# Kernel tuning notes

Measured on AMD Instinct MI355X. Metric: run time of the kernel, lower is better.

Reference implementation:

```python
import jax, jax.numpy as jnp
import numpy as np

N, M, D = 8192, 8192, 64


def setup_inputs() -> dict:
    key = jax.random.key(0)
    kx, ky = jax.random.split(key)
    X = jax.random.normal(kx, (N, D), dtype=jnp.float32)
    Y = jax.random.normal(ky, (M, D), dtype=jnp.float32)
    return {"X": X, "Y": Y}


def reference(X, Y):
    # Pairwise Euclidean distances via the |x|^2 + |y|^2 - 2<x,y> identity
    # (avoids materializing the [N, M, D] difference tensor).
    x2 = jnp.sum(X * X, axis=1)[:, None]          # [N, 1]
    y2 = jnp.sum(Y * Y, axis=1)[None, :]          # [1, M]
    d2 = x2 + y2 - 2.0 * (X @ Y.T)                # [N, M]
    d = jnp.sqrt(jnp.maximum(d2, 0.0))            # Euclidean distance matrix
    dis_1 = jnp.mean(jnp.min(d, axis=1))          # avg over X of nearest-in-Y
    dis_2 = jnp.mean(jnp.min(d, axis=0))          # avg over Y of nearest-in-X
    return dis_1 + dis_2
```

## Files before the change

### kernel.cpp

```cpp
#include <hip/hip_runtime.h>
#include <math.h>


#define NROWS 8192
#define DDIM  64
#define ITILES 64
#define SLICES 16
#define CHUNKS 4
#define LSTR 72

typedef __bf16 bf16_t;
typedef bf16_t bf16x8 __attribute__((ext_vector_type(8)));
typedef float  f32x4  __attribute__((ext_vector_type(4)));

__global__ void prep_kernel(const float* __restrict__ X,
                            const float* __restrict__ Y,
                            bf16_t* __restrict__ Xbf, bf16_t* __restrict__ Ybf,
                            float* __restrict__ x2, float* __restrict__ y2,
                            float* __restrict__ out) {
  int t = blockIdx.x * blockDim.x + threadIdx.x;
  int half = t >> 15;
  int r = (t >> 2) & (NROWS - 1);
  int part = t & 3;
  const float* src = half ? Y : X;
  bf16_t* dst = half ? Ybf : Xbf;
  float* sq = half ? y2 : x2;

  const float4* p = (const float4*)(src + r * DDIM + part * 16);
  float4 v0 = p[0], v1 = p[1], v2 = p[2], v3 = p[3];
  float s = 0.f;
  s = fmaf(v0.x, v0.x, s); s = fmaf(v0.y, v0.y, s);
  s = fmaf(v0.z, v0.z, s); s = fmaf(v0.w, v0.w, s);
  s = fmaf(v1.x, v1.x, s); s = fmaf(v1.y, v1.y, s);
  s = fmaf(v1.z, v1.z, s); s = fmaf(v1.w, v1.w, s);
  s = fmaf(v2.x, v2.x, s); s = fmaf(v2.y, v2.y, s);
  s = fmaf(v2.z, v2.z, s); s = fmaf(v2.w, v2.w, s);
  s = fmaf(v3.x, v3.x, s); s = fmaf(v3.y, v3.y, s);
  s = fmaf(v3.z, v3.z, s); s = fmaf(v3.w, v3.w, s);

  bf16x8 h0 = {(bf16_t)v0.x, (bf16_t)v0.y, (bf16_t)v0.z, (bf16_t)v0.w,
               (bf16_t)v1.x, (bf16_t)v1.y, (bf16_t)v1.z, (bf16_t)v1.w};
  bf16x8 h1 = {(bf16_t)v2.x, (bf16_t)v2.y, (bf16_t)v2.z, (bf16_t)v2.w,
               (bf16_t)v3.x, (bf16_t)v3.y, (bf16_t)v3.z, (bf16_t)v3.w};
  *(bf16x8*)&dst[r * DDIM + part * 16] = h0;
  *(bf16x8*)&dst[r * DDIM + part * 16 + 8] = h1;

  s += __shfl_xor(s, 1, 64);
  s += __shfl_xor(s, 2, 64);
  if (part == 0) sq[r] = s;
  if (t == 0) out[0] = 0.f;
}

__global__ __launch_bounds__(256, 2)
void mine_kernel(const bf16_t* __restrict__ Xbf, const bf16_t* __restrict__ Ybf,
                 const float* __restrict__ x2g, const float* __restrict__ y2g,
                 float* __restrict__ rslab, float* __restrict__ cslab) {
  __shared__ bf16_t Ys[2][128 * LSTR];

  const int tid = threadIdx.x;
  const int L = tid & 63;
  const int w = tid >> 6;
  const int lr = L & 15;
  const int q = L >> 4;
  const int rh = w >> 1;
  const int ch = w & 1;
  const int itile = blockIdx.x & (ITILES - 1);
  const int slice = blockIdx.x >> 6;
  const int i0 = itile * 128;
  const int rgb = rh * 64;
  const int cgb = ch * 64;
  const int jbase = slice * (CHUNKS * 128);

  bf16x8 Af[8];
#pragma unroll
  for (int a = 0; a < 4; ++a) {
    int row = i0 + rgb + a * 16 + lr;
#pragma unroll
    for (int h = 0; h < 2; ++h)
      Af[a * 2 + h] = *(const bf16x8*)&Xbf[row * DDIM + h * 32 + q * 8];
  }
  float x2r[16];
#pragma unroll
  for (int a = 0; a < 4; ++a) {
    float4 v = *(const float4*)&x2g[i0 + rgb + a * 16 + q * 4];
    x2r[a * 4 + 0] = v.x; x2r[a * 4 + 1] = v.y;
    x2r[a * 4 + 2] = v.z; x2r[a * 4 + 3] = v.w;
  }
  float y2all[CHUNKS][4];
#pragma unroll
  for (int cc = 0; cc < CHUNKS; ++cc)
#pragma unroll
    for (int b = 0; b < 4; ++b)
      y2all[cc][b] = y2g[jbase + cc * 128 + cgb + b * 16 + lr];

  float rmin[16];
#pragma unroll
  for (int k = 0; k < 16; ++k) rmin[k] = INFINITY;

  bf16x8 Bst[4];
#pragma unroll
  for (int p = 0; p < 4; ++p) {
    int f = p * 256 + tid;
    Bst[p] = *(const bf16x8*)&Ybf[(jbase + (f >> 3)) * DDIM + (f & 7) * 8];
  }
#pragma unroll
  for (int p = 0; p < 4; ++p) {
    int f = p * 256 + tid;
    *(bf16x8*)&Ys[0][(f >> 3) * LSTR + (f & 7) * 8] = Bst[p];
  }
  __syncthreads();

  for (int cc = 0; cc < CHUNKS; ++cc) {
    const bf16_t* Yb = Ys[cc & 1];
    if (cc + 1 < CHUNKS) {
      int j0n = jbase + (cc + 1) * 128;
#pragma unroll
      for (int p = 0; p < 4; ++p) {
        int f = p * 256 + tid;
        Bst[p] = *(const bf16x8*)&Ybf[(j0n + (f >> 3)) * DDIM + (f & 7) * 8];
      }
    }

    f32x4 acc[4][4];
#pragma unroll
    for (int a = 0; a < 4; ++a)
#pragma unroll
      for (int b = 0; b < 4; ++b) acc[a][b] = (f32x4){0.f, 0.f, 0.f, 0.f};

#pragma unroll
    for (int b = 0; b < 4; ++b) {
      bf16x8 B0 = *(const bf16x8*)&Yb[(cgb + b * 16 + lr) * LSTR + q * 8];
      bf16x8 B1 = *(const bf16x8*)&Yb[(cgb + b * 16 + lr) * LSTR + 32 + q * 8];
#pragma unroll
      for (int a = 0; a < 4; ++a) {
        acc[a][b] = __builtin_amdgcn_mfma_f32_16x16x32_bf16(Af[a * 2 + 0], B0, acc[a][b], 0, 0, 0);
        acc[a][b] = __builtin_amdgcn_mfma_f32_16x16x32_bf16(Af[a * 2 + 1], B1, acc[a][b], 0, 0, 0);
      }
    }

    float cmin[4] = {INFINITY, INFINITY, INFINITY, INFINITY};
#pragma unroll
    for (int a = 0; a < 4; ++a)
#pragma unroll
      for (int p = 0; p < 4; ++p) {
        float x2v = x2r[a * 4 + p];
        float rm = rmin[a * 4 + p];
#pragma unroll
        for (int b = 0; b < 4; ++b) {
          float s = acc[a][b][p];
          rm = fminf(rm, fmaf(-2.f, s, y2all[cc][b]));
          cmin[b] = fminf(cmin[b], fmaf(-2.f, s, x2v));
        }
        rmin[a * 4 + p] = rm;
      }
#pragma unroll
    for (int b = 0; b < 4; ++b) {
      cmin[b] = fminf(cmin[b], __shfl_xor(cmin[b], 16, 64));
      cmin[b] = fminf(cmin[b], __shfl_xor(cmin[b], 32, 64));
    }
    float v = cmin[0];
    if (q == 1) v = cmin[1];
    else if (q == 2) v = cmin[2];
    else if (q == 3) v = cmin[3];
    cslab[(itile * 2 + rh) * NROWS + jbase + cc * 128 + cgb + L] = v;

    if (cc + 1 < CHUNKS) {
      bf16_t* Yn = Ys[(cc + 1) & 1];
#pragma unroll
      for (int p = 0; p < 4; ++p) {
        int f = p * 256 + tid;
        *(bf16x8*)&Yn[(f >> 3) * LSTR + (f & 7) * 8] = Bst[p];
      }
      __syncthreads();
    }
  }

#pragma unroll
  for (int a = 0; a < 4; ++a)
#pragma unroll
    for (int p = 0; p < 4; ++p) {
      float v = rmin[a * 4 + p];
      v = fminf(v, __shfl_xor(v, 1, 64));
      v = fminf(v, __shfl_xor(v, 2, 64));
      v = fminf(v, __shfl_xor(v, 4, 64));
      v = fminf(v, __shfl_xor(v, 8, 64));
      if (lr == 0)
        rslab[slice * (NROWS * 2) + (i0 + rgb + a * 16 + q * 4 + p) * 2 + ch] = v;
    }
}

__global__ void finish_kernel(const float* __restrict__ x2,
                              const float* __restrict__ y2,
                              const float* __restrict__ rslab,
                              const float* __restrict__ cslab,
                              float* __restrict__ out) {
  const int b = blockIdx.x;
  const int tid = threadIdx.x;
  if (b < 32) {
    int row = b * 256 + tid;
    float m = INFINITY;
#pragma unroll
    for (int g = 0; g < SLICES; ++g) {
      float2 v = *(const float2*)&rslab[g * (NROWS * 2) + row * 2];
      m = fminf(m, fminf(v.x, v.y));
    }
    float v = sqrtf(fmaxf(x2[row] + m, 0.f)) * (1.0f / 8192.0f);
#pragma unroll
    for (int off = 32; off > 0; off >>= 1) v += __shfl_down(v, off, 64);
    __shared__ float partial[4];
    if ((tid & 63) == 0) partial[tid >> 6] = v;
    __syncthreads();
    if (tid == 0)
      atomicAdd(out, partial[0] + partial[1] + partial[2] + partial[3]);
  } else {
    int j = (b - 32) * 64 + (tid & 63);
    int seg = tid >> 6;
    float m = INFINITY;
#pragma unroll
    for (int k = 0; k < 32; ++k)
      m = fminf(m, cslab[(seg * 32 + k) * NROWS + j]);
    __shared__ float red[4][64];
    red[seg][tid & 63] = m;
    __syncthreads();
    if (tid < 64) {
      float mc = fminf(fminf(red[0][tid], red[1][tid]),
                       fminf(red[2][tid], red[3][tid]));
      float v = sqrtf(fmaxf(y2[j] + mc, 0.f)) * (1.0f / 8192.0f);
#pragma unroll
      for (int off = 32; off > 0; off >>= 1) v += __shfl_down(v, off, 64);
      if (tid == 0) atomicAdd(out, v);
    }
  }
}

extern "C" void kernel_launch(void* const* d_in, const int* in_sizes, int n_in,
                              void* d_out, int out_size, void* d_ws, size_t ws_size,
                              hipStream_t stream) {
  const float* X = (const float*)d_in[0];
  const float* Y = (const float*)d_in[1];
  float* out = (float*)d_out;

  char* wsb = (char*)d_ws;
  bf16_t* Xbf = (bf16_t*)wsb;
  bf16_t* Ybf = (bf16_t*)(wsb + (size_t)NROWS * DDIM * 2);
  float* x2 = (float*)(wsb + 2 * (size_t)NROWS * DDIM * 2);
  float* y2 = x2 + NROWS;
  float* rslab = y2 + NROWS;
  float* cslab = rslab + SLICES * NROWS * 2;

  prep_kernel<<<(2 * NROWS * 4) / 256, 256, 0, stream>>>(X, Y, Xbf, Ybf, x2, y2, out);
  mine_kernel<<<ITILES * SLICES, 256, 0, stream>>>(Xbf, Ybf, x2, y2, rslab, cslab);
  finish_kernel<<<160, 256, 0, stream>>>(x2, y2, rslab, cslab, out);
}
```

Measured before the change: 85.03 us.

## Fuse bf16 conversion and squared norms into the distance kernel, drop prep launch

Removes the separate prep kernel. The mine kernel now reads fp32 X and Y directly, computing the bf16 conversion and squared norms on the fly: X rows go to registers, Y chunks go to a single-buffered LDS tile plus a y2 array. Each block covers 8 column chunks instead of 4, which halves the grid to 512 blocks and halves the rslab slices. The norms are added before the slabs are written, so the finish kernel needs no x2/y2 reads. This saves a launch and the bf16/norm round trip through global memory, but loses the register-prefetch double buffering of Y and redoes the Y conversion in every i-tile block.

```diff
diff --git a/kernel.cpp b/kernel.cpp
--- a/kernel.cpp
+++ b/kernel.cpp
@@ -4,122 +4,99 @@
 
 #define NROWS 8192
 #define DDIM  64
-#define ITILES 64
-#define SLICES 16
-#define CHUNKS 4
+#define CHUNKS 8
 #define LSTR 72
 
 typedef __bf16 bf16_t;
 typedef bf16_t bf16x8 __attribute__((ext_vector_type(8)));
 typedef float  f32x4  __attribute__((ext_vector_type(4)));
 
-__global__ void prep_kernel(const float* __restrict__ X,
-                            const float* __restrict__ Y,
-                            bf16_t* __restrict__ Xbf, bf16_t* __restrict__ Ybf,
-                            float* __restrict__ x2, float* __restrict__ y2,
-                            float* __restrict__ out) {
-  int t = blockIdx.x * blockDim.x + threadIdx.x;
-  int half = t >> 15;
-  int r = (t >> 2) & (NROWS - 1);
-  int part = t & 3;
-  const float* src = half ? Y : X;
-  bf16_t* dst = half ? Ybf : Xbf;
-  float* sq = half ? y2 : x2;
-
-  const float4* p = (const float4*)(src + r * DDIM + part * 16);
-  float4 v0 = p[0], v1 = p[1], v2 = p[2], v3 = p[3];
-  float s = 0.f;
-  s = fmaf(v0.x, v0.x, s); s = fmaf(v0.y, v0.y, s);
-  s = fmaf(v0.z, v0.z, s); s = fmaf(v0.w, v0.w, s);
-  s = fmaf(v1.x, v1.x, s); s = fmaf(v1.y, v1.y, s);
-  s = fmaf(v1.z, v1.z, s); s = fmaf(v1.w, v1.w, s);
-  s = fmaf(v2.x, v2.x, s); s = fmaf(v2.y, v2.y, s);
-  s = fmaf(v2.z, v2.z, s); s = fmaf(v2.w, v2.w, s);
-  s = fmaf(v3.x, v3.x, s); s = fmaf(v3.y, v3.y, s);
-  s = fmaf(v3.z, v3.z, s); s = fmaf(v3.w, v3.w, s);
-
-  bf16x8 h0 = {(bf16_t)v0.x, (bf16_t)v0.y, (bf16_t)v0.z, (bf16_t)v0.w,
-               (bf16_t)v1.x, (bf16_t)v1.y, (bf16_t)v1.z, (bf16_t)v1.w};
-  bf16x8 h1 = {(bf16_t)v2.x, (bf16_t)v2.y, (bf16_t)v2.z, (bf16_t)v2.w,
-               (bf16_t)v3.x, (bf16_t)v3.y, (bf16_t)v3.z, (bf16_t)v3.w};
-  *(bf16x8*)&dst[r * DDIM + part * 16] = h0;
-  *(bf16x8*)&dst[r * DDIM + part * 16 + 8] = h1;
-
-  s += __shfl_xor(s, 1, 64);
-  s += __shfl_xor(s, 2, 64);
-  if (part == 0) sq[r] = s;
-  if (t == 0) out[0] = 0.f;
-}
 
 __global__ __launch_bounds__(256, 2)
-void mine_kernel(const bf16_t* __restrict__ Xbf, const bf16_t* __restrict__ Ybf,
-                 const float* __restrict__ x2g, const float* __restrict__ y2g,
-                 float* __restrict__ rslab, float* __restrict__ cslab) {
-  __shared__ bf16_t Ys[2][128 * LSTR];
+void mine_kernel(const float* __restrict__ X, const float* __restrict__ Y,
+                 float* __restrict__ rslab, float* __restrict__ cslab,
+                 float* __restrict__ out) {
+  __shared__ bf16_t Ys[128 * LSTR];
+  __shared__ float y2s[128];
 
   const int tid = threadIdx.x;
   const int L = tid & 63;
   const int w = tid >> 6;
   const int lr = L & 15;
-  const int q = L >> 4;
-  const int rh = w >> 1;
-  const int ch = w & 1;
-  const int itile = blockIdx.x & (ITILES - 1);
+  const int q  = L >> 4;
+  const int rh = w >> 1, ch = w & 1;
+  const int itile = blockIdx.x & 63;
   const int slice = blockIdx.x >> 6;
   const int i0 = itile * 128;
-  const int rgb = rh * 64;
-  const int cgb = ch * 64;
+  const int rgb = rh * 64, cgb = ch * 64;
   const int jbase = slice * (CHUNKS * 128);
 
+  if (blockIdx.x == 0 && tid == 0) out[0] = 0.f;
+
   bf16x8 Af[8];
-#pragma unroll
-  for (int a = 0; a < 4; ++a) {
-    int row = i0 + rgb + a * 16 + lr;
-#pragma unroll
-    for (int h = 0; h < 2; ++h)
-      Af[a * 2 + h] = *(const bf16x8*)&Xbf[row * DDIM + h * 32 + q * 8];
+  float x2r[16];
+  {
+    float x2acc[4];
+#pragma unroll
+    for (int a = 0; a < 4; ++a) {
+      const float4* rp = (const float4*)(X + (i0 + rgb + a * 16 + lr) * DDIM);
+      float4 u0 = rp[q * 2],     u1 = rp[q * 2 + 1];
+      float4 u2 = rp[8 + q * 2], u3 = rp[8 + q * 2 + 1];
+      float s = 0.f;
+      s = fmaf(u0.x, u0.x, s); s = fmaf(u0.y, u0.y, s);
+      s = fmaf(u0.z, u0.z, s); s = fmaf(u0.w, u0.w, s);
+      s = fmaf(u1.x, u1.x, s); s = fmaf(u1.y, u1.y, s);
+      s = fmaf(u1.z, u1.z, s); s = fmaf(u1.w, u1.w, s);
+      s = fmaf(u2.x, u2.x, s); s = fmaf(u2.y, u2.y, s);
+      s = fmaf(u2.z, u2.z, s); s = fmaf(u2.w, u2.w, s);
+      s = fmaf(u3.x, u3.x, s); s = fmaf(u3.y, u3.y, s);
+      s = fmaf(u3.z, u3.z, s); s = fmaf(u3.w, u3.w, s);
+      Af[a * 2 + 0] = (bf16x8){(bf16_t)u0.x, (bf16_t)u0.y, (bf16_t)u0.z, (bf16_t)u0.w,
+                               (bf16_t)u1.x, (bf16_t)u1.y, (bf16_t)u1.z, (bf16_t)u1.w};
+      Af[a * 2 + 1] = (bf16x8){(bf16_t)u2.x, (bf16_t)u2.y, (bf16_t)u2.z, (bf16_t)u2.w,
+                               (bf16_t)u3.x, (bf16_t)u3.y, (bf16_t)u3.z, (bf16_t)u3.w};
+      s += __shfl_xor(s, 16, 64);
+      s += __shfl_xor(s, 32, 64);
+      x2acc[a] = s;
+    }
+#pragma unroll
+    for (int a = 0; a < 4; ++a)
+#pragma unroll
+      for (int p = 0; p < 4; ++p)
+        x2r[a * 4 + p] = __shfl(x2acc[a], q * 4 + p, 64);
   }
-  float x2r[16];
-#pragma unroll
-  for (int a = 0; a < 4; ++a) {
-    float4 v = *(const float4*)&x2g[i0 + rgb + a * 16 + q * 4];
-    x2r[a * 4 + 0] = v.x; x2r[a * 4 + 1] = v.y;
-    x2r[a * 4 + 2] = v.z; x2r[a * 4 + 3] = v.w;
-  }
-  float y2all[CHUNKS][4];
-#pragma unroll
-  for (int cc = 0; cc < CHUNKS; ++cc)
-#pragma unroll
-    for (int b = 0; b < 4; ++b)
-      y2all[cc][b] = y2g[jbase + cc * 128 + cgb + b * 16 + lr];
 
   float rmin[16];
 #pragma unroll
   for (int k = 0; k < 16; ++k) rmin[k] = INFINITY;
 
-  bf16x8 Bst[4];
-#pragma unroll
-  for (int p = 0; p < 4; ++p) {
-    int f = p * 256 + tid;
-    Bst[p] = *(const bf16x8*)&Ybf[(jbase + (f >> 3)) * DDIM + (f & 7) * 8];
-  }
-#pragma unroll
-  for (int p = 0; p < 4; ++p) {
-    int f = p * 256 + tid;
-    *(bf16x8*)&Ys[0][(f >> 3) * LSTR + (f & 7) * 8] = Bst[p];
-  }
-  __syncthreads();
-
   for (int cc = 0; cc < CHUNKS; ++cc) {
-    const bf16_t* Yb = Ys[cc & 1];
-    if (cc + 1 < CHUNKS) {
-      int j0n = jbase + (cc + 1) * 128;
-#pragma unroll
-      for (int p = 0; p < 4; ++p) {
-        int f = p * 256 + tid;
-        Bst[p] = *(const bf16x8*)&Ybf[(j0n + (f >> 3)) * DDIM + (f & 7) * 8];
-      }
-    }
+    const int j0 = jbase + cc * 128;
+    __syncthreads();
+#pragma unroll
+    for (int p = 0; p < 4; ++p) {
+      int f = p * 256 + tid;
+      int r = f >> 3, c = f & 7;
+      const float4* yp = (const float4*)(Y + (j0 + r) * DDIM);
+      float4 a0 = yp[c * 2], a1 = yp[c * 2 + 1];
+      float s = 0.f;
+      s = fmaf(a0.x, a0.x, s); s = fmaf(a0.y, a0.y, s);
+      s = fmaf(a0.z, a0.z, s); s = fmaf(a0.w, a0.w, s);
+      s = fmaf(a1.x, a1.x, s); s = fmaf(a1.y, a1.y, s);
+      s = fmaf(a1.z, a1.z, s); s = fmaf(a1.w, a1.w, s);
+      s += __shfl_xor(s, 1, 64);
+      s += __shfl_xor(s, 2, 64);
+      s += __shfl_xor(s, 4, 64);
+      if ((tid & 7) == 0) y2s[r] = s;
+      bf16x8 hv = {(bf16_t)a0.x, (bf16_t)a0.y, (bf16_t)a0.z, (bf16_t)a0.w,
+                   (bf16_t)a1.x, (bf16_t)a1.y, (bf16_t)a1.z, (bf16_t)a1.w};
+      *(bf16x8*)&Ys[r * LSTR + c * 8] = hv;
+    }
+    __syncthreads();
+
+    float y2c[4];
+#pragma unroll
+    for (int b = 0; b < 4; ++b) y2c[b] = y2s[cgb + b * 16 + lr];
 
     f32x4 acc[4][4];
 #pragma unroll
@@ -129,8 +106,8 @@
 
 #pragma unroll
     for (int b = 0; b < 4; ++b) {
-      bf16x8 B0 = *(const bf16x8*)&Yb[(cgb + b * 16 + lr) * LSTR + q * 8];
-      bf16x8 B1 = *(const bf16x8*)&Yb[(cgb + b * 16 + lr) * LSTR + 32 + q * 8];
+      bf16x8 B0 = *(const bf16x8*)&Ys[(cgb + b * 16 + lr) * LSTR + q * 8];
+      bf16x8 B1 = *(const bf16x8*)&Ys[(cgb + b * 16 + lr) * LSTR + 32 + q * 8];
 #pragma unroll
       for (int a = 0; a < 4; ++a) {
         acc[a][b] = __builtin_amdgcn_mfma_f32_16x16x32_bf16(Af[a * 2 + 0], B0, acc[a][b], 0, 0, 0);
@@ -144,35 +121,27 @@
 #pragma unroll
       for (int p = 0; p < 4; ++p) {
         float x2v = x2r[a * 4 + p];
-        float rm = rmin[a * 4 + p];
-#pragma unroll
-        for (int b = 0; b < 4; ++b) {
-          float s = acc[a][b][p];
-          rm = fminf(rm, fmaf(-2.f, s, y2all[cc][b]));
-          cmin[b] = fminf(cmin[b], fmaf(-2.f, s, x2v));
-        }
-        rmin[a * 4 + p] = rm;
+        float t0 = fmaf(-2.f, acc[a][0][p], y2c[0]);
+        float t1 = fmaf(-2.f, acc[a][1][p], y2c[1]);
+        float t2 = fmaf(-2.f, acc[a][2][p], y2c[2]);
+        float t3 = fmaf(-2.f, acc[a][3][p], y2c[3]);
+        rmin[a * 4 + p] = fminf(rmin[a * 4 + p],
+                                fminf(fminf(t0, t1), fminf(t2, t3)));
+        cmin[0] = fminf(cmin[0], fmaf(-2.f, acc[a][0][p], x2v));
+        cmin[1] = fminf(cmin[1], fmaf(-2.f, acc[a][1][p], x2v));
+        cmin[2] = fminf(cmin[2], fmaf(-2.f, acc[a][2][p], x2v));
+        cmin[3] = fminf(cmin[3], fmaf(-2.f, acc[a][3][p], x2v));
       }
 #pragma unroll
     for (int b = 0; b < 4; ++b) {
       cmin[b] = fminf(cmin[b], __shfl_xor(cmin[b], 16, 64));
       cmin[b] = fminf(cmin[b], __shfl_xor(cmin[b], 32, 64));
     }
-    float v = cmin[0];
-    if (q == 1) v = cmin[1];
-    else if (q == 2) v = cmin[2];
-    else if (q == 3) v = cmin[3];
-    cslab[(itile * 2 + rh) * NROWS + jbase + cc * 128 + cgb + L] = v;
-
-    if (cc + 1 < CHUNKS) {
-      bf16_t* Yn = Ys[(cc + 1) & 1];
-#pragma unroll
-      for (int p = 0; p < 4; ++p) {
-        int f = p * 256 + tid;
-        *(bf16x8*)&Yn[(f >> 3) * LSTR + (f & 7) * 8] = Bst[p];
-      }
-      __syncthreads();
-    }
+    float v = cmin[0], yv = y2c[0];
+    if (q == 1) { v = cmin[1]; yv = y2c[1]; }
+    else if (q == 2) { v = cmin[2]; yv = y2c[2]; }
+    else if (q == 3) { v = cmin[3]; yv = y2c[3]; }
+    cslab[(itile * 2 + rh) * NROWS + j0 + cgb + L] = v + yv;
   }
 
 #pragma unroll
@@ -185,13 +154,12 @@
       v = fminf(v, __shfl_xor(v, 4, 64));
       v = fminf(v, __shfl_xor(v, 8, 64));
       if (lr == 0)
-        rslab[slice * (NROWS * 2) + (i0 + rgb + a * 16 + q * 4 + p) * 2 + ch] = v;
+        rslab[slice * (NROWS * 2) + (i0 + rgb + a * 16 + q * 4 + p) * 2 + ch] =
+            v + x2r[a * 4 + p];
     }
 }
 
-__global__ void finish_kernel(const float* __restrict__ x2,
-                              const float* __restrict__ y2,
-                              const float* __restrict__ rslab,
+__global__ void finish_kernel(const float* __restrict__ rslab,
                               const float* __restrict__ cslab,
                               float* __restrict__ out) {
   const int b = blockIdx.x;
@@ -200,11 +168,11 @@
     int row = b * 256 + tid;
     float m = INFINITY;
 #pragma unroll
-    for (int g = 0; g < SLICES; ++g) {
+    for (int g = 0; g < 8; ++g) {
       float2 v = *(const float2*)&rslab[g * (NROWS * 2) + row * 2];
       m = fminf(m, fminf(v.x, v.y));
     }
-    float v = sqrtf(fmaxf(x2[row] + m, 0.f)) * (1.0f / 8192.0f);
+    float v = sqrtf(fmaxf(m, 0.f)) * (1.0f / 8192.0f);
 #pragma unroll
     for (int off = 32; off > 0; off >>= 1) v += __shfl_down(v, off, 64);
     __shared__ float partial[4];
@@ -225,7 +193,7 @@
     if (tid < 64) {
       float mc = fminf(fminf(red[0][tid], red[1][tid]),
                        fminf(red[2][tid], red[3][tid]));
-      float v = sqrtf(fmaxf(y2[j] + mc, 0.f)) * (1.0f / 8192.0f);
+      float v = sqrtf(fmaxf(mc, 0.f)) * (1.0f / 8192.0f);
 #pragma unroll
       for (int off = 32; off > 0; off >>= 1) v += __shfl_down(v, off, 64);
       if (tid == 0) atomicAdd(out, v);
@@ -240,15 +208,9 @@
   const float* Y = (const float*)d_in[1];
   float* out = (float*)d_out;
 
-  char* wsb = (char*)d_ws;
-  bf16_t* Xbf = (bf16_t*)wsb;
-  bf16_t* Ybf = (bf16_t*)(wsb + (size_t)NROWS * DDIM * 2);
-  float* x2 = (float*)(wsb + 2 * (size_t)NROWS * DDIM * 2);
-  float* y2 = x2 + NROWS;
-  float* rslab = y2 + NROWS;
-  float* cslab = rslab + SLICES * NROWS * 2;
-
-  prep_kernel<<<(2 * NROWS * 4) / 256, 256, 0, stream>>>(X, Y, Xbf, Ybf, x2, y2, out);
-  mine_kernel<<<ITILES * SLICES, 256, 0, stream>>>(Xbf, Ybf, x2, y2, rslab, cslab);
-  finish_kernel<<<160, 256, 0, stream>>>(x2, y2, rslab, cslab, out);
+  float* rslab = (float*)d_ws;
+  float* cslab = rslab + 8 * NROWS * 2;
+
+  mine_kernel<<<512, 256, 0, stream>>>(X, Y, rslab, cslab, out);
+  finish_kernel<<<160, 256, 0, stream>>>(rslab, cslab, out);
 }
```

Result: slower. 89.27 us (+5.0%).

## Fuse finish reduction into mine kernel via last-block ticket counter

Applied to the files above, without the earlier changes.

Removes the separate finish kernel launch. Each mine block takes a ticket from an atomic counter, and the last 16 blocks spin until all blocks are done, then each reduces one shard of rows and columns and atomically adds to the output. The x2/y2 norms are now folded into the slab values at write time, so the tail does not reload them. This saves a kernel launch and its gap in exchange for a spin-wait and a serialized tail over only 16 blocks, with a deadlock risk if those blocks become resident before all the others finish.

```diff
diff --git a/kernel.cpp b/kernel.cpp
--- a/kernel.cpp
+++ b/kernel.cpp
@@ -8,15 +8,19 @@
 #define SLICES 16
 #define CHUNKS 4
 #define LSTR 72
+#define GRID (ITILES * SLICES)
+#define TAILS 16
 
 typedef __bf16 bf16_t;
 typedef bf16_t bf16x8 __attribute__((ext_vector_type(8)));
 typedef float  f32x4  __attribute__((ext_vector_type(4)));
+
 
 __global__ void prep_kernel(const float* __restrict__ X,
                             const float* __restrict__ Y,
                             bf16_t* __restrict__ Xbf, bf16_t* __restrict__ Ybf,
                             float* __restrict__ x2, float* __restrict__ y2,
+                            unsigned* __restrict__ counter,
                             float* __restrict__ out) {
   int t = blockIdx.x * blockDim.x + threadIdx.x;
   int half = t >> 15;
@@ -48,27 +52,28 @@
   s += __shfl_xor(s, 1, 64);
   s += __shfl_xor(s, 2, 64);
   if (part == 0) sq[r] = s;
-  if (t == 0) out[0] = 0.f;
+  if (t == 0) { out[0] = 0.f; *counter = 0u; }
 }
 
 __global__ __launch_bounds__(256, 2)
 void mine_kernel(const bf16_t* __restrict__ Xbf, const bf16_t* __restrict__ Ybf,
                  const float* __restrict__ x2g, const float* __restrict__ y2g,
-                 float* __restrict__ rslab, float* __restrict__ cslab) {
+                 float* __restrict__ rslab, float* __restrict__ cslab,
+                 unsigned* __restrict__ counter, float* __restrict__ out) {
   __shared__ bf16_t Ys[2][128 * LSTR];
+  __shared__ unsigned ticket_s;
+  __shared__ float partial[4];
 
   const int tid = threadIdx.x;
   const int L = tid & 63;
   const int w = tid >> 6;
   const int lr = L & 15;
-  const int q = L >> 4;
-  const int rh = w >> 1;
-  const int ch = w & 1;
+  const int q  = L >> 4;
+  const int rh = w >> 1, ch = w & 1;
   const int itile = blockIdx.x & (ITILES - 1);
   const int slice = blockIdx.x >> 6;
   const int i0 = itile * 128;
-  const int rgb = rh * 64;
-  const int cgb = ch * 64;
+  const int rgb = rh * 64, cgb = ch * 64;
   const int jbase = slice * (CHUNKS * 128);
 
   bf16x8 Af[8];
@@ -158,11 +163,11 @@
       cmin[b] = fminf(cmin[b], __shfl_xor(cmin[b], 16, 64));
       cmin[b] = fminf(cmin[b], __shfl_xor(cmin[b], 32, 64));
     }
-    float v = cmin[0];
-    if (q == 1) v = cmin[1];
-    else if (q == 2) v = cmin[2];
-    else if (q == 3) v = cmin[3];
-    cslab[(itile * 2 + rh) * NROWS + jbase + cc * 128 + cgb + L] = v;
+    float v = cmin[0], yv = y2all[cc][0];
+    if (q == 1) { v = cmin[1]; yv = y2all[cc][1]; }
+    else if (q == 2) { v = cmin[2]; yv = y2all[cc][2]; }
+    else if (q == 3) { v = cmin[3]; yv = y2all[cc][3]; }
+    cslab[(itile * 2 + rh) * NROWS + jbase + cc * 128 + cgb + L] = v + yv;
 
     if (cc + 1 < CHUNKS) {
       bf16_t* Yn = Ys[(cc + 1) & 1];
@@ -185,52 +190,55 @@
       v = fminf(v, __shfl_xor(v, 4, 64));
       v = fminf(v, __shfl_xor(v, 8, 64));
       if (lr == 0)
-        rslab[slice * (NROWS * 2) + (i0 + rgb + a * 16 + q * 4 + p) * 2 + ch] = v;
-    }
-}
-
-__global__ void finish_kernel(const float* __restrict__ x2,
-                              const float* __restrict__ y2,
-                              const float* __restrict__ rslab,
-                              const float* __restrict__ cslab,
-                              float* __restrict__ out) {
-  const int b = blockIdx.x;
-  const int tid = threadIdx.x;
-  if (b < 32) {
-    int row = b * 256 + tid;
+        rslab[slice * (NROWS * 2) + (i0 + rgb + a * 16 + q * 4 + p) * 2 + ch] =
+            v + x2r[a * 4 + p];
+    }
+
+  __threadfence();
+  __syncthreads();
+  if (tid == 0)
+    ticket_s = __hip_atomic_fetch_add(counter, 1u, __ATOMIC_ACQ_REL,
+                                      __HIP_MEMORY_SCOPE_AGENT);
+  __syncthreads();
+  const unsigned ticket = ticket_s;
+  if (ticket < GRID - TAILS) return;
+
+  if (tid == 0) {
+    while (__hip_atomic_load(counter, __ATOMIC_ACQUIRE,
+                             __HIP_MEMORY_SCOPE_AGENT) < GRID)
+      __builtin_amdgcn_s_sleep(8);
+  }
+  __syncthreads();
+  __threadfence();
+
+  const int shard = (int)(ticket - (GRID - TAILS));
+  float sum = 0.f;
+#pragma unroll
+  for (int rr = 0; rr < 2; ++rr) {
+    int row = shard * 512 + rr * 256 + tid;
     float m = INFINITY;
 #pragma unroll
     for (int g = 0; g < SLICES; ++g) {
       float2 v = *(const float2*)&rslab[g * (NROWS * 2) + row * 2];
       m = fminf(m, fminf(v.x, v.y));
     }
-    float v = sqrtf(fmaxf(x2[row] + m, 0.f)) * (1.0f / 8192.0f);
-#pragma unroll
-    for (int off = 32; off > 0; off >>= 1) v += __shfl_down(v, off, 64);
-    __shared__ float partial[4];
-    if ((tid & 63) == 0) partial[tid >> 6] = v;
-    __syncthreads();
-    if (tid == 0)
-      atomicAdd(out, partial[0] + partial[1] + partial[2] + partial[3]);
-  } else {
-    int j = (b - 32) * 64 + (tid & 63);
-    int seg = tid >> 6;
+    sum += sqrtf(fmaxf(m, 0.f));
+  }
+#pragma unroll
+  for (int jj = 0; jj < 2; ++jj) {
+    int j = shard * 512 + jj * 256 + tid;
     float m = INFINITY;
-#pragma unroll
-    for (int k = 0; k < 32; ++k)
-      m = fminf(m, cslab[(seg * 32 + k) * NROWS + j]);
-    __shared__ float red[4][64];
-    red[seg][tid & 63] = m;
-    __syncthreads();
-    if (tid < 64) {
-      float mc = fminf(fminf(red[0][tid], red[1][tid]),
-                       fminf(red[2][tid], red[3][tid]));
-      float v = sqrtf(fmaxf(y2[j] + mc, 0.f)) * (1.0f / 8192.0f);
-#pragma unroll
-      for (int off = 32; off > 0; off >>= 1) v += __shfl_down(v, off, 64);
-      if (tid == 0) atomicAdd(out, v);
-    }
-  }
+#pragma unroll 8
+    for (int p = 0; p < 128; ++p) m = fminf(m, cslab[p * NROWS + j]);
+    sum += sqrtf(fmaxf(m, 0.f));
+  }
+  sum *= (1.0f / 8192.0f);
+#pragma unroll
+  for (int off = 32; off > 0; off >>= 1) sum += __shfl_down(sum, off, 64);
+  if ((tid & 63) == 0) partial[tid >> 6] = sum;
+  __syncthreads();
+  if (tid == 0)
+    atomicAdd(out, partial[0] + partial[1] + partial[2] + partial[3]);
 }
 
 extern "C" void kernel_launch(void* const* d_in, const int* in_sizes, int n_in,
@@ -247,8 +255,8 @@
   float* y2 = x2 + NROWS;
   float* rslab = y2 + NROWS;
   float* cslab = rslab + SLICES * NROWS * 2;
-
-  prep_kernel<<<(2 * NROWS * 4) / 256, 256, 0, stream>>>(X, Y, Xbf, Ybf, x2, y2, out);
-  mine_kernel<<<ITILES * SLICES, 256, 0, stream>>>(Xbf, Ybf, x2, y2, rslab, cslab);
-  finish_kernel<<<160, 256, 0, stream>>>(x2, y2, rslab, cslab, out);
+  unsigned* counter = (unsigned*)(cslab + 128 * NROWS);
+
+  prep_kernel<<<(2 * NROWS * 4) / 256, 256, 0, stream>>>(X, Y, Xbf, Ybf, x2, y2, counter, out);
+  mine_kernel<<<GRID, 256, 0, stream>>>(Xbf, Ybf, x2, y2, rslab, cslab, counter, out);
 }
```

Result: slower. 231.8 us (+172.6%).
